# Kernel tuning notes

Measured on AMD Instinct MI355X. Metric: run time of the kernel, lower is better.

## Reference

```python
import jax, jax.numpy as jnp
import numpy as np

B, S, D = 2, 2048, 2048
H, G = 16, 4
HD = D // H          # head_dim = 128
KV = HD * G          # 512


def setup_inputs() -> dict:
    key = jax.random.key(0)
    ks = jax.random.split(key, 5)
    scale = 1.0 / np.sqrt(D)
    return {
        "x": jax.random.normal(ks[0], (B, S, D), dtype=jnp.float32),
        "Wqkv": jax.random.normal(ks[1], (D, D + 2 * KV), dtype=jnp.float32) * scale,
        "bqkv": jax.random.normal(ks[2], (D + 2 * KV,), dtype=jnp.float32) * 0.01,
        "Wout": jax.random.normal(ks[3], (D, D), dtype=jnp.float32) * scale,
        "bout": jax.random.normal(ks[4], (D,), dtype=jnp.float32) * 0.01,
    }


def reference(x, Wqkv, bqkv, Wout, bout):
    b, s, _ = x.shape
    qkv = x @ Wqkv + bqkv                                  # [b, s, D + 2*KV]
    q, k, v = jnp.split(qkv, [D, D + KV], axis=-1)
    q = q.reshape(b, s, H, HD)                             # [b, s, H, hd]
    # torch .repeat tiles the group axis: head h -> group (h % G)
    k = jnp.tile(k.reshape(b, s, G, HD), (1, 1, H // G, 1))  # [b, s, H, hd]
    v = jnp.tile(v.reshape(b, s, G, HD), (1, 1, H // G, 1))
    # NOTE: original divides by head_dim (not sqrt(head_dim)) -- kept faithfully
    scores = jnp.einsum("bqhd,bkhd->bhqk", q, k) / HD      # [b, H, s, s]
    prob = jax.nn.softmax(scores, axis=-1)
    out = jnp.einsum("bhqk,bkhd->bqhd", prob, v).reshape(b, s, D)
    return out @ Wout + bout
```

## Files before the change

kernel.cpp:

```cpp
#include <hip/hip_runtime.h>
#include <stdint.h>

typedef __bf16 bf16;
typedef __bf16 bf16x8 __attribute__((ext_vector_type(8)));
typedef __bf16 bf16x4 __attribute__((ext_vector_type(4)));
typedef float  f32x4  __attribute__((ext_vector_type(4)));

#define B_   2
#define S_   2048
#define D_   2048
#define H_   16
#define G_   4
#define HD_  128
#define KV_  512
#define NQKV 3072
#define M_   4096

__device__ __forceinline__ void async16(bf16* lds, const bf16* g) {
  __builtin_amdgcn_global_load_lds(
      (const __attribute__((address_space(1))) unsigned int*)g,
      (__attribute__((address_space(3))) unsigned int*)lds, 16, 0, 0);
}

__device__ __forceinline__ f32x4 mfma16(bf16x8 a, bf16x8 b, f32x4 c) {
  return __builtin_amdgcn_mfma_f32_16x16x32_bf16(a, b, c, 0, 0, 0);
}

__global__ __launch_bounds__(256) void prep_kernel(const float* __restrict__ x,
                                                   const float* __restrict__ Wqkv,
                                                   const float* __restrict__ Wout,
                                                   bf16* __restrict__ xb,
                                                   bf16* __restrict__ wqkvT,
                                                   bf16* __restrict__ woutT) {
  __shared__ float tile[32][33];
  int bid = blockIdx.x;
  int t = threadIdx.x;

  if (bid < 8192) {
    int i = bid * 256 + t;
    float4 v = ((const float4*)x)[i];
    bf16x4 o = { (bf16)v.x, (bf16)v.y, (bf16)v.z, (bf16)v.w };
    *(bf16x4*)(xb + (size_t)i * 4) = o;
    return;
  }
  bid -= 8192;

  const float* src; bf16* dst; int rows, cols, nct;
  if (bid < 6144) { src = Wqkv; dst = wqkvT; rows = 2048; cols = 3072; nct = 96; }
  else { bid -= 6144; src = Wout; dst = woutT; rows = 2048; cols = 2048; nct = 64; }

  int bc = (bid % nct) * 32, br = (bid / nct) * 32;
  int tx = t & 31, ty = t >> 5;
  #pragma unroll
  for (int i = 0; i < 32; i += 8)
    tile[ty + i][tx] = src[(size_t)(br + ty + i) * cols + bc + tx];
  __syncthreads();
  #pragma unroll
  for (int i = 0; i < 32; i += 8)
    dst[(size_t)(bc + ty + i) * rows + br + tx] = (bf16)tile[tx][ty + i];
}

__global__ void transpose_v_kernel(const bf16* __restrict__ qkv,
                                   bf16* __restrict__ vt) {
  __shared__ bf16 tile[32][33];
  int bg = blockIdx.z; int b = bg / G_, g = bg % G_;
  int sb = blockIdx.x * 32, db = blockIdx.y * 32;
  int tx = threadIdx.x, ty = threadIdx.y;
  const bf16* src = qkv + (size_t)b * S_ * NQKV + (D_ + KV_ + g * HD_);
  #pragma unroll
  for (int i = 0; i < 32; i += 8)
    tile[ty + i][tx] = src[(size_t)(sb + ty + i) * NQKV + db + tx];
  __syncthreads();
  bf16* dst = vt + (size_t)(b * G_ + g) * HD_ * S_;
  int txp = ((tx & 15) >> 2) * 8 + (tx >> 4) * 4 + (tx & 3);
  #pragma unroll
  for (int i = 0; i < 32; i += 8)
    dst[(size_t)(db + ty + i) * S_ + sb + txp] = tile[tx][ty + i];
}

template <int OUT_BF16>
__global__ __launch_bounds__(256) void gemm_bt(const bf16* __restrict__ A,
                                               const bf16* __restrict__ Bt,
                                               const float* __restrict__ bias,
                                               void* __restrict__ Cout,
                                               int Ndim, int K) {
  __shared__ __align__(16) bf16 As[128 * 32];
  __shared__ __align__(16) bf16 Bs[128 * 32];
  int t = threadIdx.x;
  int w = t >> 6, l = t & 63, lr = l & 15, lg = l >> 4;
  int wm = w >> 1, wn = w & 1;
  int row0 = blockIdx.x * 128, col0 = blockIdx.y * 128;

  f32x4 acc[4][4] = {};

  const bf16* ga = A  + (size_t)(row0 + (t >> 2)) * K + (t & 3) * 8;
  const bf16* gb = Bt + (size_t)(col0 + (t >> 2)) * K + (t & 3) * 8;

  for (int k0 = 0; k0 < K; k0 += 32) {
    __syncthreads();
    #pragma unroll
    for (int i = 0; i < 2; i++)
      async16(&As[w * 512 + i * 2048], ga + (size_t)i * 64 * K + k0);
    #pragma unroll
    for (int i = 0; i < 2; i++)
      async16(&Bs[w * 512 + i * 2048], gb + (size_t)i * 64 * K + k0);
    __syncthreads();

    bf16x8 af[4], bfr[4];
    #pragma unroll
    for (int mi = 0; mi < 4; mi++)
      af[mi] = *(const bf16x8*)&As[(wm * 64 + mi * 16 + lr) * 32 + lg * 8];
    #pragma unroll
    for (int ni = 0; ni < 4; ni++)
      bfr[ni] = *(const bf16x8*)&Bs[(wn * 64 + ni * 16 + lr) * 32 + lg * 8];
    #pragma unroll
    for (int mi = 0; mi < 4; mi++)
      #pragma unroll
      for (int ni = 0; ni < 4; ni++)
        acc[mi][ni] = mfma16(af[mi], bfr[ni], acc[mi][ni]);
  }

  float bv[4];
  #pragma unroll
  for (int ni = 0; ni < 4; ni++)
    bv[ni] = bias[col0 + wn * 64 + ni * 16 + lr];

  #pragma unroll
  for (int mi = 0; mi < 4; mi++)
    #pragma unroll
    for (int ni = 0; ni < 4; ni++)
      #pragma unroll
      for (int r = 0; r < 4; r++) {
        int row = row0 + wm * 64 + mi * 16 + lg * 4 + r;
        int col = col0 + wn * 64 + ni * 16 + lr;
        float v = acc[mi][ni][r] + bv[ni];
        if (OUT_BF16)
          ((bf16*)Cout)[(size_t)row * Ndim + col] = (bf16)v;
        else
          ((float*)Cout)[(size_t)row * Ndim + col] = v;
      }
}

__global__ __launch_bounds__(256, 2) void attn_kernel(const bf16* __restrict__ qkv,
                                                      const bf16* __restrict__ vt,
                                                      bf16* __restrict__ attnb) {
  __shared__ __align__(16) bf16 Ks[2][64 * 128];
  __shared__ __align__(16) bf16 Vs[2][128 * 64];

  int t = threadIdx.x, w = t >> 6, l = t & 63, lr = l & 15, lg = l >> 4;
  int rsw = lr & 7;
  int lin = blockIdx.x + gridDim.x * blockIdx.y;
  int swz = (lin & 7) * 64 + (lin >> 3);
  int q0 = (swz & 15) * 128;
  int hb2 = swz >> 4;
  int b = hb2 >> 4, gh = hb2 & 15;
  int g = gh >> 2, h = (gh & 3) * 4 + g;

  bf16x8 qf[2][4];
  #pragma unroll
  for (int mi = 0; mi < 2; mi++) {
    const bf16* qbase = qkv + (size_t)(b * S_ + q0 + w * 32 + mi * 16 + lr) * NQKV + h * HD_;
    #pragma unroll
    for (int kc = 0; kc < 4; kc++)
      qf[mi][kc] = *(const bf16x8*)(qbase + kc * 32 + lg * 8);
  }

  const bf16* kbase = qkv + (size_t)b * S_ * NQKV + D_ + g * HD_;
  const bf16* vbase = vt + (size_t)(b * G_ + g) * HD_ * S_;

  int krowi = w * 4 + (l >> 4);
  int ksw = (l & 15) ^ (krowi & 7);
  const bf16* kgl = kbase + (size_t)krowi * NQKV + ksw * 8;
  int vrowi = w * 8 + (l >> 3);
  int vsw = (l & 7) ^ ((l >> 3) & 7);
  const bf16* vgl = vbase + (size_t)vrowi * S_ + vsw * 8;

  auto STAGE_KV = [&](int nb, int kv0) {
    #pragma unroll
    for (int i = 0; i < 4; i++)
      async16(&Ks[nb][w * 512 + i * 2048], kgl + (size_t)(kv0 + i * 16) * NQKV);
    #pragma unroll
    for (int i = 0; i < 4; i++)
      async16(&Vs[nb][w * 512 + i * 2048], vgl + (size_t)(i * 32) * S_ + kv0);
  };

  float lsump[2] = {};
  f32x4 accO[2][8] = {};

  STAGE_KV(0, 0);

  for (int ti = 0; ti < S_ / 64; ++ti) {
    int cur = ti & 1;
    int kv0 = ti * 64;
    __syncthreads();
    if (ti + 1 < S_ / 64) STAGE_KV(cur ^ 1, kv0 + 64);

    const bf16* ks = &Ks[cur][0];
    const bf16* vs = &Vs[cur][0];

    bf16x8 pa[2][2];
    __builtin_amdgcn_s_setprio(1);
    #pragma unroll
    for (int fk = 0; fk < 4; fk++) {
      bf16x8 kf[4];
      #pragma unroll
      for (int kc = 0; kc < 4; kc++)
        kf[kc] = *(const bf16x8*)&ks[(fk * 16 + lr) * 128 + (((kc * 4 + lg) ^ rsw) * 8)];
      f32x4 sacc[2] = {};
      #pragma unroll
      for (int mi = 0; mi < 2; mi++)
        #pragma unroll
        for (int kc = 0; kc < 4; kc++)
          sacc[mi] = mfma16(kf[kc], qf[mi][kc], sacc[mi]);
      #pragma unroll
      for (int mi = 0; mi < 2; mi++) {
        float p0 = __expf(sacc[mi][0] * 0.0078125f);
        float p1 = __expf(sacc[mi][1] * 0.0078125f);
        float p2 = __expf(sacc[mi][2] * 0.0078125f);
        float p3 = __expf(sacc[mi][3] * 0.0078125f);
        lsump[mi] += (p0 + p1) + (p2 + p3);
        pa[mi][fk >> 1][(fk & 1) * 4 + 0] = (bf16)p0;
        pa[mi][fk >> 1][(fk & 1) * 4 + 1] = (bf16)p1;
        pa[mi][fk >> 1][(fk & 1) * 4 + 2] = (bf16)p2;
        pa[mi][fk >> 1][(fk & 1) * 4 + 3] = (bf16)p3;
      }
    }

    #pragma unroll
    for (int fd = 0; fd < 8; fd++) {
      bf16x8 vfr[2];
      #pragma unroll
      for (int kk = 0; kk < 2; kk++)
        vfr[kk] = *(const bf16x8*)&vs[(fd * 16 + lr) * 64 + (((kk * 4 + lg) ^ rsw) * 8)];
      #pragma unroll
      for (int mi = 0; mi < 2; mi++)
        #pragma unroll
        for (int kk = 0; kk < 2; kk++)
          accO[mi][fd] = mfma16(pa[mi][kk], vfr[kk], accO[mi][fd]);
    }
    __builtin_amdgcn_s_setprio(0);
  }

  #pragma unroll
  for (int mi = 0; mi < 2; mi++) {
    float s = lsump[mi];
    s += __shfl_xor(s, 16);
    s += __shfl_xor(s, 32);
    float rls[4];
    #pragma unroll
    for (int r = 0; r < 4; r++) rls[r] = 1.f / __shfl(s, lg * 4 + r);
    bf16* obase = attnb + (size_t)(b * S_ + q0 + w * 32 + mi * 16) * D_ + h * HD_;
    #pragma unroll
    for (int r = 0; r < 4; r++)
      #pragma unroll
      for (int fd = 0; fd < 8; fd++)
        obase[(size_t)(lg * 4 + r) * D_ + fd * 16 + lr] =
            (bf16)(accO[mi][fd][r] * rls[r]);
  }
}

extern "C" void kernel_launch(void* const* d_in, const int* in_sizes, int n_in,
                              void* d_out, int out_size, void* d_ws, size_t ws_size,
                              hipStream_t stream) {
  const float* x    = (const float*)d_in[0];
  const float* Wqkv = (const float*)d_in[1];
  const float* bqkv = (const float*)d_in[2];
  const float* Wout = (const float*)d_in[3];
  const float* bout = (const float*)d_in[4];
  float* out = (float*)d_out;

  char* p = (char*)d_ws;
  bf16* xb    = (bf16*)p; p += (size_t)M_ * D_ * 2;
  bf16* wqkvT = (bf16*)p; p += (size_t)NQKV * D_ * 2;
  bf16* woutT = (bf16*)p; p += (size_t)D_ * D_ * 2;
  bf16* qkvb  = (bf16*)p; p += (size_t)M_ * NQKV * 2;
  bf16* vtb   = (bf16*)p; p += (size_t)B_ * G_ * HD_ * S_ * 2;
  bf16* attnb = (bf16*)p; p += (size_t)M_ * D_ * 2;

  prep_kernel<<<dim3(8192 + 6144 + 4096), dim3(256), 0, stream>>>(
      x, Wqkv, Wout, xb, wqkvT, woutT);

  gemm_bt<1><<<dim3(M_ / 128, NQKV / 128), dim3(256), 0, stream>>>(xb, wqkvT, bqkv, (void*)qkvb, NQKV, D_);

  transpose_v_kernel<<<dim3(S_ / 32, HD_ / 32, B_ * G_), dim3(32, 8), 0, stream>>>(qkvb, vtb);

  attn_kernel<<<dim3(S_ / 128, B_ * H_), dim3(256), 0, stream>>>(qkvb, vtb, attnb);

  gemm_bt<0><<<dim3(M_ / 128, D_ / 128), dim3(256), 0, stream>>>(attnb, woutT, bout, (void*)out, D_, D_);
}
```

Before: 210.9 us.

## Software-pipeline attention loop: overlap previous PV with current QK^T via triple-buffered V

```diff
diff --git a/kernel.cpp b/kernel.cpp
--- a/kernel.cpp
+++ b/kernel.cpp
@@ -145,7 +145,7 @@
                                                       const bf16* __restrict__ vt,
                                                       bf16* __restrict__ attnb) {
   __shared__ __align__(16) bf16 Ks[2][64 * 128];
-  __shared__ __align__(16) bf16 Vs[2][128 * 64];
+  __shared__ __align__(16) bf16 Vs[3][128 * 64];
 
   int t = threadIdx.x, w = t >> 6, l = t & 63, lr = l & 15, lg = l >> 4;
   int rsw = lr & 7;
@@ -175,71 +175,107 @@
   int vsw = (l & 7) ^ ((l >> 3) & 7);
   const bf16* vgl = vbase + (size_t)vrowi * S_ + vsw * 8;
 
-  auto STAGE_KV = [&](int nb, int kv0) {
+  auto STAGE_K = [&](int nb, int kv0) {
     #pragma unroll
     for (int i = 0; i < 4; i++)
       async16(&Ks[nb][w * 512 + i * 2048], kgl + (size_t)(kv0 + i * 16) * NQKV);
+  };
+  auto STAGE_V = [&](bf16* vb, int kv0) {
     #pragma unroll
     for (int i = 0; i < 4; i++)
-      async16(&Vs[nb][w * 512 + i * 2048], vgl + (size_t)(i * 32) * S_ + kv0);
+      async16(&vb[w * 512 + i * 2048], vgl + (size_t)(i * 32) * S_ + kv0);
   };
 
   float lsump[2] = {};
   f32x4 accO[2][8] = {};
-
-  STAGE_KV(0, 0);
-
-  for (int ti = 0; ti < S_ / 64; ++ti) {
-    int cur = ti & 1;
-    int kv0 = ti * 64;
-    __syncthreads();
-    if (ti + 1 < S_ / 64) STAGE_KV(cur ^ 1, kv0 + 64);
-
-    const bf16* ks = &Ks[cur][0];
-    const bf16* vs = &Vs[cur][0];
-
-    bf16x8 pa[2][2];
-    __builtin_amdgcn_s_setprio(1);
-    #pragma unroll
-    for (int fk = 0; fk < 4; fk++) {
-      bf16x8 kf[4];
-      #pragma unroll
-      for (int kc = 0; kc < 4; kc++)
-        kf[kc] = *(const bf16x8*)&ks[(fk * 16 + lr) * 128 + (((kc * 4 + lg) ^ rsw) * 8)];
-      f32x4 sacc[2] = {};
-      #pragma unroll
-      for (int mi = 0; mi < 2; mi++)
-        #pragma unroll
-        for (int kc = 0; kc < 4; kc++)
-          sacc[mi] = mfma16(kf[kc], qf[mi][kc], sacc[mi]);
-      #pragma unroll
-      for (int mi = 0; mi < 2; mi++) {
-        float p0 = __expf(sacc[mi][0] * 0.0078125f);
-        float p1 = __expf(sacc[mi][1] * 0.0078125f);
-        float p2 = __expf(sacc[mi][2] * 0.0078125f);
-        float p3 = __expf(sacc[mi][3] * 0.0078125f);
-        lsump[mi] += (p0 + p1) + (p2 + p3);
-        pa[mi][fk >> 1][(fk & 1) * 4 + 0] = (bf16)p0;
-        pa[mi][fk >> 1][(fk & 1) * 4 + 1] = (bf16)p1;
-        pa[mi][fk >> 1][(fk & 1) * 4 + 2] = (bf16)p2;
-        pa[mi][fk >> 1][(fk & 1) * 4 + 3] = (bf16)p3;
-      }
-    }
-
-    #pragma unroll
-    for (int fd = 0; fd < 8; fd++) {
-      bf16x8 vfr[2];
-      #pragma unroll
-      for (int kk = 0; kk < 2; kk++)
-        vfr[kk] = *(const bf16x8*)&vs[(fd * 16 + lr) * 64 + (((kk * 4 + lg) ^ rsw) * 8)];
-      #pragma unroll
-      for (int mi = 0; mi < 2; mi++)
-        #pragma unroll
-        for (int kk = 0; kk < 2; kk++)
-          accO[mi][fd] = mfma16(pa[mi][kk], vfr[kk], accO[mi][fd]);
-    }
-    __builtin_amdgcn_s_setprio(0);
-  }
+  bf16x8 paA[2][2], paB[2][2];
+
+#define QKT_BLOCK(KSBUF, PAC)                                                \
+  {                                                                          \
+    const bf16* ks = (KSBUF);                                                \
+    __builtin_amdgcn_s_setprio(1);                                           \
+    _Pragma("unroll")                                                        \
+    for (int fk = 0; fk < 4; fk++) {                                         \
+      bf16x8 kf[4];                                                          \
+      _Pragma("unroll")                                                      \
+      for (int kc = 0; kc < 4; kc++)                                         \
+        kf[kc] = *(const bf16x8*)&ks[(fk * 16 + lr) * 128 +                  \
+                                     (((kc * 4 + lg) ^ rsw) * 8)];           \
+      f32x4 sacc[2] = {};                                                    \
+      _Pragma("unroll")                                                      \
+      for (int mi = 0; mi < 2; mi++)                                         \
+        _Pragma("unroll")                                                    \
+        for (int kc = 0; kc < 4; kc++)                                       \
+          sacc[mi] = mfma16(kf[kc], qf[mi][kc], sacc[mi]);                   \
+      _Pragma("unroll")                                                      \
+      for (int mi = 0; mi < 2; mi++) {                                       \
+        float p0 = __expf(sacc[mi][0] * 0.0078125f);                         \
+        float p1 = __expf(sacc[mi][1] * 0.0078125f);                         \
+        float p2 = __expf(sacc[mi][2] * 0.0078125f);                         \
+        float p3 = __expf(sacc[mi][3] * 0.0078125f);                         \
+        lsump[mi] += (p0 + p1) + (p2 + p3);                                  \
+        PAC[mi][fk >> 1][(fk & 1) * 4 + 0] = (bf16)p0;                       \
+        PAC[mi][fk >> 1][(fk & 1) * 4 + 1] = (bf16)p1;                       \
+        PAC[mi][fk >> 1][(fk & 1) * 4 + 2] = (bf16)p2;                       \
+        PAC[mi][fk >> 1][(fk & 1) * 4 + 3] = (bf16)p3;                       \
+      }                                                                      \
+    }                                                                        \
+    __builtin_amdgcn_s_setprio(0);                                           \
+  }
+
+#define PV_BLOCK(PAP, VSBUF)                                                 \
+  {                                                                          \
+    const bf16* vsp = (VSBUF);                                               \
+    __builtin_amdgcn_s_setprio(1);                                           \
+    _Pragma("unroll")                                                        \
+    for (int fd = 0; fd < 8; fd++) {                                         \
+      bf16x8 vfr[2];                                                         \
+      _Pragma("unroll")                                                      \
+      for (int kk = 0; kk < 2; kk++)                                         \
+        vfr[kk] = *(const bf16x8*)&vsp[(fd * 16 + lr) * 64 +                 \
+                                       (((kk * 4 + lg) ^ rsw) * 8)];         \
+      _Pragma("unroll")                                                      \
+      for (int mi = 0; mi < 2; mi++)                                         \
+        _Pragma("unroll")                                                    \
+        for (int kk = 0; kk < 2; kk++)                                       \
+          accO[mi][fd] = mfma16(PAP[mi][kk], vfr[kk], accO[mi][fd]);         \
+    }                                                                        \
+    __builtin_amdgcn_s_setprio(0);                                           \
+  }
+
+#define BODY(TI, PAP, PAC, VPREV, VNEXT)                                     \
+  {                                                                          \
+    __syncthreads();                                                         \
+    if ((TI) + 1 < S_ / 64) {                                                \
+      STAGE_K(((TI) + 1) & 1, ((TI) + 1) * 64);                              \
+      STAGE_V((VNEXT), ((TI) + 1) * 64);                                     \
+    }                                                                        \
+    PV_BLOCK(PAP, VPREV);                                                    \
+    QKT_BLOCK(&Ks[(TI) & 1][0], PAC);                                        \
+  }
+
+  STAGE_K(0, 0);
+  STAGE_V(&Vs[0][0], 0);
+  __syncthreads();
+  STAGE_K(1, 64);
+  STAGE_V(&Vs[1][0], 64);
+  QKT_BLOCK(&Ks[0][0], paA);
+
+  bf16* vp = &Vs[0][0];
+  bf16* vc = &Vs[1][0];
+  bf16* vn = &Vs[2][0];
+
+  for (int ti = 1; ti < 31; ti += 2) {
+    BODY(ti,     paA, paB, vp, vn);
+    BODY(ti + 1, paB, paA, vc, vp);
+    bf16* tmp = vp; vp = vn; vn = vc; vc = tmp;
+  }
+  BODY(31, paA, paB, vp, vn);
+  PV_BLOCK(paB, vc);
+
+#undef QKT_BLOCK
+#undef PV_BLOCK
+#undef BODY
 
   #pragma unroll
   for (int mi = 0; mi < 2; mi++) {
```

After: 210.8 us. Within noise of the previous version (-0.1%).
